# Performance work log

Hardware: AMD Instinct MI355X
Metric: run time of the kernel (lower is better)

The kernel has to match this reference:

```python
import jax, jax.numpy as jnp
import numpy as np

N, D_IN, D_OUT, BATCH = 64, 512, 512, 1024


def setup_inputs() -> dict:
    key = jax.random.key(0)
    kx, kw, kb = jax.random.split(key, 3)
    x = jax.random.normal(kx, (BATCH, N, D_IN), dtype=jnp.float32)
    # nn.Linear-style init: U(-1/sqrt(d_in), 1/sqrt(d_in)); weight stored transposed (n, d_in, d_out)
    bound = 1.0 / np.sqrt(D_IN)
    weight = jax.random.uniform(kw, (N, D_IN, D_OUT), minval=-bound, maxval=bound, dtype=jnp.float32)
    bias = jax.random.uniform(kb, (N, D_OUT), minval=-bound, maxval=bound, dtype=jnp.float32)
    return {"x": x, "weight": weight, "bias": bias}


def reference(x, weight, bias):
    # Same math as (x[..., None] * weight[None]).sum(-2) + bias[None],
    # expressed as a batched GEMM over the n independent linear layers.
    out = jnp.einsum("bni,nio->bno", x, weight)  # (batch, n, d_out)
    return out + bias[None]
```

## Files before the change

### kernel.cpp

```cpp
#include <hip/hip_runtime.h>
#include <hip/hip_bf16.h>

#define NL    64
#define DIN   512
#define DOUT  512
#define BATCH 1024

#define BM 256
#define BN 256
#define BK 32
#define NK (DIN / BK)
#define LDS_STRIDE 40

typedef short short8 __attribute__((ext_vector_type(8)));
typedef float f32x4  __attribute__((ext_vector_type(4)));

__device__ __forceinline__ unsigned int pk2(float a, float b) {
    __hip_bfloat162 h = __float22bfloat162_rn(make_float2(a, b));
    unsigned int r;
    __builtin_memcpy(&r, &h, 4);
    return r;
}

__global__ __launch_bounds__(512, 2) void nlinear_kernel(
        const float* __restrict__ x, const float* __restrict__ w,
        const float* __restrict__ bias, float* __restrict__ out) {
    __shared__ unsigned short As[2][BM * LDS_STRIDE];
    __shared__ unsigned short Bs[2][BN * LDS_STRIDE];

    const int tid = threadIdx.x;
    const int bid = blockIdx.x;
    const int nb    = (bid & 7) * 64 + (bid >> 3);
    const int layer = nb >> 3;
    const int t     = nb & 7;
    const int bm0   = (t & 3) * BM;
    const int bn0   = (t >> 2) * BN;

    const int wid  = tid >> 6;
    const int lane = tid & 63;
    const int wr   = wid >> 2, wc = wid & 3;
    const int lrow = lane & 15;
    const int lkb  = lane >> 4;

    const int ar = tid >> 3;
    const int ak = tid & 7;
    const int gw = tid >> 6;
    const int gc = tid & 63;

    const size_t XS = (size_t)NL * DIN;
    const float* xb = x + (size_t)bm0 * XS + (size_t)layer * DIN;
    const float* wb = w + (size_t)layer * DIN * DOUT + bn0;
    const float* aptr0 = xb + (size_t)ar * XS + ak * 4;
    const float* bptr0 = wb + (size_t)(gw * 4) * DOUT + gc * 4;

    f32x4 acc[8][4];
#pragma unroll
    for (int i = 0; i < 8; ++i)
#pragma unroll
        for (int j = 0; j < 4; ++j) acc[i][j] = (f32x4){0.f, 0.f, 0.f, 0.f};

    f32x4 av[4], bv[4];

    auto issue = [&](int kt) {
#pragma unroll
        for (int p = 0; p < 4; ++p)
            av[p] = *reinterpret_cast<const f32x4*>(
                aptr0 + (size_t)(64 * p) * XS + kt * BK);
#pragma unroll
        for (int p = 0; p < 4; ++p)
            bv[p] = *reinterpret_cast<const f32x4*>(
                bptr0 + (size_t)(kt * BK + p) * DOUT);
    };

    auto cvtwrite = [&](int b) {
#pragma unroll
        for (int p = 0; p < 4; ++p) {
            uint2 wv;
            wv.x = pk2(av[p][0], av[p][1]);
            wv.y = pk2(av[p][2], av[p][3]);
            *reinterpret_cast<uint2*>(
                &As[b][(ar + 64 * p) * LDS_STRIDE + ak * 4]) = wv;
        }
#pragma unroll
        for (int j = 0; j < 4; ++j) {
            const int col = gc * 4 + j;
            uint2 wv;
            wv.x = pk2(bv[0][j], bv[1][j]);
            wv.y = pk2(bv[2][j], bv[3][j]);
            *reinterpret_cast<uint2*>(
                &Bs[b][col * LDS_STRIDE + gw * 4]) = wv;
        }
    };

    auto fragA = [&](int b, short8* af) {
#pragma unroll
        for (int mi = 0; mi < 8; ++mi) {
            const int row = wr * 128 + mi * 16 + lrow;
            af[mi] = *reinterpret_cast<const short8*>(
                &As[b][row * LDS_STRIDE + lkb * 8]);
        }
    };
    auto fragB = [&](int b, short8* bf) {
#pragma unroll
        for (int ni = 0; ni < 4; ++ni) {
            const int col = wc * 64 + ni * 16 + lrow;
            bf[ni] = *reinterpret_cast<const short8*>(
                &Bs[b][col * LDS_STRIDE + lkb * 8]);
        }
    };

#define BARRIER() do { \
        asm volatile("s_waitcnt lgkmcnt(0)" ::: "memory"); \
        __builtin_amdgcn_sched_barrier(0); \
        __builtin_amdgcn_s_barrier(); \
        __builtin_amdgcn_sched_barrier(0); } while (0)

#define MFMA32(AF, BF) do { \
        __builtin_amdgcn_s_setprio(1); \
        _Pragma("unroll") \
        for (int mi = 0; mi < 8; ++mi) \
        _Pragma("unroll") \
            for (int ni = 0; ni < 4; ++ni) \
                acc[mi][ni] = __builtin_amdgcn_mfma_f32_16x16x32_bf16( \
                    AF[mi], BF[ni], acc[mi][ni], 0, 0, 0); \
        __builtin_amdgcn_s_setprio(0); } while (0)

    issue(0);
    cvtwrite(0);
    issue(1);
    BARRIER();

#pragma unroll 1
    for (int k = 0; k < NK - 2; ++k) {
        short8 af[8], bf[4];
        fragA(k & 1, af);
        fragB(k & 1, bf);
        cvtwrite((k + 1) & 1);
        issue(k + 2);
        MFMA32(af, bf);
        BARRIER();
    }
    {
        short8 af[8], bf[4];
        fragA((NK - 2) & 1, af);
        fragB((NK - 2) & 1, bf);
        cvtwrite((NK - 1) & 1);
        MFMA32(af, bf);
        BARRIER();
    }
    {
        short8 af[8], bf[4];
        fragA((NK - 1) & 1, af);
        fragB((NK - 1) & 1, bf);
        MFMA32(af, bf);
    }

    const float* bb = bias + (size_t)layer * DOUT + bn0;
    float* ob = out + (size_t)bm0 * (NL * DOUT) + (size_t)layer * DOUT + bn0;
#pragma unroll
    for (int mi = 0; mi < 8; ++mi) {
#pragma unroll
        for (int ni = 0; ni < 4; ++ni) {
            const int col = wc * 64 + ni * 16 + lrow;
            const float bval = bb[col];
#pragma unroll
            for (int r = 0; r < 4; ++r) {
                const int row = wr * 128 + mi * 16 + lkb * 4 + r;
                ob[(size_t)row * (NL * DOUT) + col] = acc[mi][ni][r] + bval;
            }
        }
    }
#undef BARRIER
#undef MFMA32
}

extern "C" void kernel_launch(void* const* d_in, const int* in_sizes, int n_in,
                              void* d_out, int out_size, void* d_ws, size_t ws_size,
                              hipStream_t stream) {
    const float* x  = (const float*)d_in[0];
    const float* w  = (const float*)d_in[1];
    const float* b  = (const float*)d_in[2];
    float* out      = (float*)d_out;

    dim3 grid(NL * (BATCH / BM) * (DOUT / BN));
    dim3 block(512);
    hipLaunchKernelGGL(nlinear_kernel, grid, block, 0, stream, x, w, b, out);
}
```

Baseline: 93.18 us.

## Use BK=64 tiles with XOR-swizzled LDS and four-phase interleaved MFMA pipeline

```diff
diff --git a/kernel.cpp b/kernel.cpp
--- a/kernel.cpp
+++ b/kernel.cpp
@@ -8,9 +8,8 @@
 
 #define BM 256
 #define BN 256
-#define BK 32
-#define NK (DIN / BK)
-#define LDS_STRIDE 40
+#define BK 64
+#define NT (DIN / BK)
 
 typedef short short8 __attribute__((ext_vector_type(8)));
 typedef float f32x4  __attribute__((ext_vector_type(4)));
@@ -25,16 +24,17 @@
 __global__ __launch_bounds__(512, 2) void nlinear_kernel(
         const float* __restrict__ x, const float* __restrict__ w,
         const float* __restrict__ bias, float* __restrict__ out) {
-    __shared__ unsigned short As[2][BM * LDS_STRIDE];
-    __shared__ unsigned short Bs[2][BN * LDS_STRIDE];
+    extern __shared__ unsigned short lds[];
+    unsigned short* const Abuf = lds;
+    unsigned short* const Bbuf = lds + 2 * BM * BK;
 
     const int tid = threadIdx.x;
     const int bid = blockIdx.x;
     const int nb    = (bid & 7) * 64 + (bid >> 3);
     const int layer = nb >> 3;
-    const int t     = nb & 7;
-    const int bm0   = (t & 3) * BM;
-    const int bn0   = (t >> 2) * BN;
+    const int t8    = nb & 7;
+    const int bm0   = (t8 & 3) * BM;
+    const int bn0   = (t8 >> 2) * BN;
 
     const int wid  = tid >> 6;
     const int lane = tid & 63;
@@ -43,15 +43,15 @@
     const int lkb  = lane >> 4;
 
     const int ar = tid >> 3;
-    const int ak = tid & 7;
-    const int gw = tid >> 6;
-    const int gc = tid & 63;
+    const int ac = tid & 7;
+    const int kq = tid & 15;
+    const int cg = tid >> 4;
 
     const size_t XS = (size_t)NL * DIN;
     const float* xb = x + (size_t)bm0 * XS + (size_t)layer * DIN;
     const float* wb = w + (size_t)layer * DIN * DOUT + bn0;
-    const float* aptr0 = xb + (size_t)ar * XS + ak * 4;
-    const float* bptr0 = wb + (size_t)(gw * 4) * DOUT + gc * 4;
+    const float* aptr = xb + (size_t)ar * XS + ac * 8;
+    const float* bptr = wb + (size_t)(kq * 4) * DOUT + cg * 8;
 
     f32x4 acc[8][4];
 #pragma unroll
@@ -59,119 +59,152 @@
 #pragma unroll
         for (int j = 0; j < 4; ++j) acc[i][j] = (f32x4){0.f, 0.f, 0.f, 0.f};
 
-    f32x4 av[4], bv[4];
-
-    auto issue = [&](int kt) {
-#pragma unroll
-        for (int p = 0; p < 4; ++p)
-            av[p] = *reinterpret_cast<const f32x4*>(
-                aptr0 + (size_t)(64 * p) * XS + kt * BK);
-#pragma unroll
-        for (int p = 0; p < 4; ++p)
-            bv[p] = *reinterpret_cast<const f32x4*>(
-                bptr0 + (size_t)(kt * BK + p) * DOUT);
-    };
-
-    auto cvtwrite = [&](int b) {
-#pragma unroll
-        for (int p = 0; p < 4; ++p) {
+    f32x4 avr[4][2];
+    f32x4 bvr[4][2];
+
+    auto issueA = [&](int t) {
+#pragma unroll
+        for (int j = 0; j < 4; ++j) {
+            const float* p = aptr + (size_t)(64 * j) * XS + t * BK;
+            avr[j][0] = *reinterpret_cast<const f32x4*>(p);
+            avr[j][1] = *reinterpret_cast<const f32x4*>(p + 4);
+        }
+    };
+    auto issueB = [&](int t) {
+#pragma unroll
+        for (int ki = 0; ki < 4; ++ki) {
+            const float* p = bptr + (size_t)(t * BK + ki) * DOUT;
+            bvr[ki][0] = *reinterpret_cast<const f32x4*>(p);
+            bvr[ki][1] = *reinterpret_cast<const f32x4*>(p + 4);
+        }
+    };
+    auto cvtwriteA = [&](int db, int p) {
+        unsigned short* dst = Abuf + db * (BM * BK);
+#pragma unroll
+        for (int jj = 0; jj < 2; ++jj) {
+            const int j = 2 * p + jj;
+            const int r = ar + 64 * j;
+            uint4 wv;
+            wv.x = pk2(avr[j][0][0], avr[j][0][1]);
+            wv.y = pk2(avr[j][0][2], avr[j][0][3]);
+            wv.z = pk2(avr[j][1][0], avr[j][1][1]);
+            wv.w = pk2(avr[j][1][2], avr[j][1][3]);
+            *reinterpret_cast<uint4*>(&dst[r * BK + ((ac ^ (r & 7)) << 3)]) = wv;
+        }
+    };
+    auto cvtwriteB = [&](int db, int p) {
+        unsigned short* dst = Bbuf + db * (BN * BK);
+#pragma unroll
+        for (int jj = 0; jj < 4; ++jj) {
+            const int j = 4 * p + jj;
+            const int c = cg * 8 + j;
+            const int h = j >> 2, e = j & 3;
             uint2 wv;
-            wv.x = pk2(av[p][0], av[p][1]);
-            wv.y = pk2(av[p][2], av[p][3]);
-            *reinterpret_cast<uint2*>(
-                &As[b][(ar + 64 * p) * LDS_STRIDE + ak * 4]) = wv;
-        }
-#pragma unroll
-        for (int j = 0; j < 4; ++j) {
-            const int col = gc * 4 + j;
-            uint2 wv;
-            wv.x = pk2(bv[0][j], bv[1][j]);
-            wv.y = pk2(bv[2][j], bv[3][j]);
-            *reinterpret_cast<uint2*>(
-                &Bs[b][col * LDS_STRIDE + gw * 4]) = wv;
-        }
-    };
-
-    auto fragA = [&](int b, short8* af) {
-#pragma unroll
-        for (int mi = 0; mi < 8; ++mi) {
-            const int row = wr * 128 + mi * 16 + lrow;
+            wv.x = pk2(bvr[0][h][e], bvr[1][h][e]);
+            wv.y = pk2(bvr[2][h][e], bvr[3][h][e]);
+            const int off = c * BK + (((kq >> 1) ^ (c & 7)) << 3) + ((kq & 1) << 2);
+            *reinterpret_cast<uint2*>(&dst[off]) = wv;
+        }
+    };
+
+    auto fragA = [&](int db, int kh, int mh, short8* af) {
+        const unsigned short* src = Abuf + db * (BM * BK);
+#pragma unroll
+        for (int mi = 0; mi < 4; ++mi) {
+            const int row = wr * 128 + mh * 64 + mi * 16 + lrow;
+            const int s = kh * 4 + lkb;
             af[mi] = *reinterpret_cast<const short8*>(
-                &As[b][row * LDS_STRIDE + lkb * 8]);
-        }
-    };
-    auto fragB = [&](int b, short8* bf) {
+                &src[row * BK + ((s ^ (row & 7)) << 3)]);
+        }
+    };
+    auto fragB = [&](int db, int kh, short8* bf) {
+        const unsigned short* src = Bbuf + db * (BN * BK);
 #pragma unroll
         for (int ni = 0; ni < 4; ++ni) {
             const int col = wc * 64 + ni * 16 + lrow;
+            const int s = kh * 4 + lkb;
             bf[ni] = *reinterpret_cast<const short8*>(
-                &Bs[b][col * LDS_STRIDE + lkb * 8]);
-        }
-    };
-
-#define BARRIER() do { \
+                &src[col * BK + ((s ^ (col & 7)) << 3)]);
+        }
+    };
+
+#define PHASE_SYNC_PRE() do { \
+        __builtin_amdgcn_s_barrier(); \
         asm volatile("s_waitcnt lgkmcnt(0)" ::: "memory"); \
+        __builtin_amdgcn_sched_barrier(0); } while (0)
+#define PHASE_SYNC_POST() do { \
         __builtin_amdgcn_sched_barrier(0); \
-        __builtin_amdgcn_s_barrier(); \
-        __builtin_amdgcn_sched_barrier(0); } while (0)
-
-#define MFMA32(AF, BF) do { \
+        __builtin_amdgcn_s_barrier(); } while (0)
+
+#define MFMA16(MH, AF, BF) do { \
         __builtin_amdgcn_s_setprio(1); \
         _Pragma("unroll") \
-        for (int mi = 0; mi < 8; ++mi) \
+        for (int mi = 0; mi < 4; ++mi) \
         _Pragma("unroll") \
             for (int ni = 0; ni < 4; ++ni) \
-                acc[mi][ni] = __builtin_amdgcn_mfma_f32_16x16x32_bf16( \
-                    AF[mi], BF[ni], acc[mi][ni], 0, 0, 0); \
+                acc[(MH) * 4 + mi][ni] = __builtin_amdgcn_mfma_f32_16x16x32_bf16( \
+                    AF[mi], BF[ni], acc[(MH) * 4 + mi][ni], 0, 0, 0); \
         __builtin_amdgcn_s_setprio(0); } while (0)
 
-    issue(0);
-    cvtwrite(0);
-    issue(1);
-    BARRIER();
+    issueA(0); issueB(0);
+    cvtwriteA(0, 0); cvtwriteA(0, 1);
+    cvtwriteB(0, 0); cvtwriteB(0, 1);
+    issueA(1); issueB(1);
+    asm volatile("s_waitcnt lgkmcnt(0)" ::: "memory");
+    __builtin_amdgcn_sched_barrier(0);
+    __builtin_amdgcn_s_barrier();
 
 #pragma unroll 1
-    for (int k = 0; k < NK - 2; ++k) {
-        short8 af[8], bf[4];
-        fragA(k & 1, af);
-        fragB(k & 1, bf);
-        cvtwrite((k + 1) & 1);
-        issue(k + 2);
-        MFMA32(af, bf);
-        BARRIER();
-    }
-    {
-        short8 af[8], bf[4];
-        fragA((NK - 2) & 1, af);
-        fragB((NK - 2) & 1, bf);
-        cvtwrite((NK - 1) & 1);
-        MFMA32(af, bf);
-        BARRIER();
-    }
-    {
-        short8 af[8], bf[4];
-        fragA((NK - 1) & 1, af);
-        fragB((NK - 1) & 1, bf);
-        MFMA32(af, bf);
+    for (int t = 0; t < NT; ++t) {
+        const int cur = t & 1, oth = cur ^ 1;
+        short8 af[4], bf[4];
+
+        fragB(cur, 0, bf);
+        fragA(cur, 0, 0, af);
+        if (t < NT - 1) { cvtwriteA(oth, 0); cvtwriteB(oth, 0); }
+        PHASE_SYNC_PRE();
+        MFMA16(0, af, bf);
+        PHASE_SYNC_POST();
+
+        fragA(cur, 0, 1, af);
+        if (t < NT - 1) { cvtwriteA(oth, 1); cvtwriteB(oth, 1); }
+        PHASE_SYNC_PRE();
+        MFMA16(1, af, bf);
+        PHASE_SYNC_POST();
+
+        fragB(cur, 1, bf);
+        fragA(cur, 1, 0, af);
+        if (t < NT - 2) issueA(t + 2);
+        PHASE_SYNC_PRE();
+        MFMA16(0, af, bf);
+        PHASE_SYNC_POST();
+
+        fragA(cur, 1, 1, af);
+        if (t < NT - 2) issueB(t + 2);
+        PHASE_SYNC_PRE();
+        MFMA16(1, af, bf);
+        PHASE_SYNC_POST();
     }
 
     const float* bb = bias + (size_t)layer * DOUT + bn0;
     float* ob = out + (size_t)bm0 * (NL * DOUT) + (size_t)layer * DOUT + bn0;
 #pragma unroll
-    for (int mi = 0; mi < 8; ++mi) {
+    for (int m8 = 0; m8 < 8; ++m8) {
 #pragma unroll
         for (int ni = 0; ni < 4; ++ni) {
             const int col = wc * 64 + ni * 16 + lrow;
             const float bval = bb[col];
 #pragma unroll
             for (int r = 0; r < 4; ++r) {
-                const int row = wr * 128 + mi * 16 + lkb * 4 + r;
-                ob[(size_t)row * (NL * DOUT) + col] = acc[mi][ni][r] + bval;
+                const int row = wr * 128 + (m8 >> 2) * 64 + (m8 & 3) * 16
+                              + lkb * 4 + r;
+                ob[(size_t)row * (NL * DOUT) + col] = acc[m8][ni][r] + bval;
             }
         }
     }
-#undef BARRIER
-#undef MFMA32
+#undef PHASE_SYNC_PRE
+#undef PHASE_SYNC_POST
+#undef MFMA16
 }
 
 extern "C" void kernel_launch(void* const* d_in, const int* in_sizes, int n_in,
@@ -182,7 +215,13 @@
     const float* b  = (const float*)d_in[2];
     float* out      = (float*)d_out;
 
+    static const size_t lds_bytes = 2 * (size_t)(BM * BK + BN * BK) * 2;
+    hipFuncSetAttribute((const void*)nlinear_kernel,
+                        hipFuncAttributeMaxDynamicSharedMemorySize,
+                        (int)lds_bytes);
+
     dim3 grid(NL * (BATCH / BM) * (DOUT / BN));
     dim3 block(512);
-    hipLaunchKernelGGL(nlinear_kernel, grid, block, 0, stream, x, w, b, out);
+    hipLaunchKernelGGL(nlinear_kernel, grid, block, lds_bytes, stream,
+                       x, w, b, out);
 }
```

New measurement: 116.9 us. +25.5%, slower.

## Deepen A-tile global prefetch and XOR-swizzle B tile in shared memory

Applied to the files above, without the earlier changes.

```diff
diff --git a/kernel.cpp b/kernel.cpp
--- a/kernel.cpp
+++ b/kernel.cpp
@@ -10,7 +10,7 @@
 #define BN 256
 #define BK 32
 #define NK (DIN / BK)
-#define LDS_STRIDE 40
+#define LDSS 40
 
 typedef short short8 __attribute__((ext_vector_type(8)));
 typedef float f32x4  __attribute__((ext_vector_type(4)));
@@ -25,16 +25,16 @@
 __global__ __launch_bounds__(512, 2) void nlinear_kernel(
         const float* __restrict__ x, const float* __restrict__ w,
         const float* __restrict__ bias, float* __restrict__ out) {
-    __shared__ unsigned short As[2][BM * LDS_STRIDE];
-    __shared__ unsigned short Bs[2][BN * LDS_STRIDE];
+    __shared__ unsigned short As[2][BM * LDSS];
+    __shared__ unsigned short Bs[2][BN * LDSS];
 
     const int tid = threadIdx.x;
     const int bid = blockIdx.x;
     const int nb    = (bid & 7) * 64 + (bid >> 3);
     const int layer = nb >> 3;
-    const int t     = nb & 7;
-    const int bm0   = (t & 3) * BM;
-    const int bn0   = (t >> 2) * BN;
+    const int t8    = nb & 7;
+    const int bm0   = (t8 & 3) * BM;
+    const int bn0   = (t8 >> 2) * BN;
 
     const int wid  = tid >> 6;
     const int lane = tid & 63;
@@ -59,53 +59,65 @@
 #pragma unroll
         for (int j = 0; j < 4; ++j) acc[i][j] = (f32x4){0.f, 0.f, 0.f, 0.f};
 
-    f32x4 av[4], bv[4];
-
-    auto issue = [&](int kt) {
+    f32x4 avE[4], avO[4];
+    f32x4 bv[4];
+
+    auto issueA = [&](int kt, f32x4 (&s)[4]) {
 #pragma unroll
         for (int p = 0; p < 4; ++p)
-            av[p] = *reinterpret_cast<const f32x4*>(
+            s[p] = *reinterpret_cast<const f32x4*>(
                 aptr0 + (size_t)(64 * p) * XS + kt * BK);
+    };
+    auto issueB = [&](int kt) {
 #pragma unroll
         for (int p = 0; p < 4; ++p)
             bv[p] = *reinterpret_cast<const f32x4*>(
                 bptr0 + (size_t)(kt * BK + p) * DOUT);
     };
 
-    auto cvtwrite = [&](int b) {
+    auto cvtwriteA = [&](int db, f32x4 (&s)[4]) {
 #pragma unroll
         for (int p = 0; p < 4; ++p) {
             uint2 wv;
-            wv.x = pk2(av[p][0], av[p][1]);
-            wv.y = pk2(av[p][2], av[p][3]);
+            wv.x = pk2(s[p][0], s[p][1]);
+            wv.y = pk2(s[p][2], s[p][3]);
             *reinterpret_cast<uint2*>(
-                &As[b][(ar + 64 * p) * LDS_STRIDE + ak * 4]) = wv;
-        }
+                &As[db][(ar + 64 * p) * LDSS + ak * 4]) = wv;
+        }
+    };
+    auto cvtwriteB = [&](int db) {
 #pragma unroll
         for (int j = 0; j < 4; ++j) {
-            const int col = gc * 4 + j;
+            const int c = gc * 4 + j;
             uint2 wv;
             wv.x = pk2(bv[0][j], bv[1][j]);
             wv.y = pk2(bv[2][j], bv[3][j]);
+            const int slot = gw ^ ((c >> 2) & 7);
             *reinterpret_cast<uint2*>(
-                &Bs[b][col * LDS_STRIDE + gw * 4]) = wv;
-        }
-    };
-
-    auto fragA = [&](int b, short8* af) {
+                &Bs[db][c * LDSS + slot * 4]) = wv;
+        }
+    };
+
+    auto fragA = [&](int db, short8* af) {
 #pragma unroll
         for (int mi = 0; mi < 8; ++mi) {
             const int row = wr * 128 + mi * 16 + lrow;
             af[mi] = *reinterpret_cast<const short8*>(
-                &As[b][row * LDS_STRIDE + lkb * 8]);
-        }
-    };
-    auto fragB = [&](int b, short8* bf) {
+                &As[db][row * LDSS + lkb * 8]);
+        }
+    };
+    auto fragB = [&](int db, short8* bf) {
 #pragma unroll
         for (int ni = 0; ni < 4; ++ni) {
             const int col = wc * 64 + ni * 16 + lrow;
-            bf[ni] = *reinterpret_cast<const short8*>(
-                &Bs[b][col * LDS_STRIDE + lkb * 8]);
+            const int key = (col >> 2) & 7;
+            const unsigned short* base = &Bs[db][col * LDSS];
+            uint2 lo = *reinterpret_cast<const uint2*>(
+                base + (((2 * lkb) ^ key) << 2));
+            uint2 hi = *reinterpret_cast<const uint2*>(
+                base + (((2 * lkb + 1) ^ key) << 2));
+            uint4 u = make_uint4(lo.x, lo.y, hi.x, hi.y);
+            __builtin_memcpy(&bf[ni], &u, 16);
         }
     };
 
@@ -125,33 +137,53 @@
                     AF[mi], BF[ni], acc[mi][ni], 0, 0, 0); \
         __builtin_amdgcn_s_setprio(0); } while (0)
 
-    issue(0);
-    cvtwrite(0);
-    issue(1);
+    issueA(0, avE);
+    issueB(0);
+    cvtwriteA(0, avE);
+    cvtwriteB(0);
+    issueA(1, avO);
+    issueB(1);
+    issueA(2, avE);
     BARRIER();
 
 #pragma unroll 1
-    for (int k = 0; k < NK - 2; ++k) {
+    for (int k = 0; k < NK - 2; k += 2) {
+        {
+            short8 af[8], bf[4];
+            fragA(0, af);
+            fragB(0, bf);
+            cvtwriteA(1, avO);
+            cvtwriteB(1);
+            issueA(k + 3, avO);
+            issueB(k + 2);
+            MFMA32(af, bf);
+            BARRIER();
+        }
+        {
+            short8 af[8], bf[4];
+            fragA(1, af);
+            fragB(1, bf);
+            cvtwriteA(0, avE);
+            cvtwriteB(0);
+            if (k + 4 < NK) issueA(k + 4, avE);
+            issueB(k + 3);
+            MFMA32(af, bf);
+            BARRIER();
+        }
+    }
+    {
         short8 af[8], bf[4];
-        fragA(k & 1, af);
-        fragB(k & 1, bf);
-        cvtwrite((k + 1) & 1);
-        issue(k + 2);
+        fragA(0, af);
+        fragB(0, bf);
+        cvtwriteA(1, avO);
+        cvtwriteB(1);
         MFMA32(af, bf);
         BARRIER();
     }
     {
         short8 af[8], bf[4];
-        fragA((NK - 2) & 1, af);
-        fragB((NK - 2) & 1, bf);
-        cvtwrite((NK - 1) & 1);
-        MFMA32(af, bf);
-        BARRIER();
-    }
-    {
-        short8 af[8], bf[4];
-        fragA((NK - 1) & 1, af);
-        fragB((NK - 1) & 1, bf);
+        fragA(1, af);
+        fragB(1, bf);
         MFMA32(af, bf);
     }
 
```

Result: no change. 93.11 us (-0.1%).
